# Performance work log

Measured on AMD Instinct MI355X. Metric: run time of the kernel, lower is better.

## Reference

```python
import jax, jax.numpy as jnp
import numpy as np

B, S, H, NH = 2, 2048, 1024, 16
HD = H // NH
INV_NORM = 1.0 / float(np.sqrt(HD))
BETA = 1.0


def setup_inputs() -> dict:
    key = jax.random.key(0)
    ks = jax.random.split(key, 8)
    causal = ~jnp.tril(jnp.ones((S, S), dtype=bool))  # True = masked (future)
    return {
        "hidden_states": jax.random.normal(ks[0], (B, S, H), dtype=jnp.float32),
        "residual": jax.random.normal(ks[1], (B, S, H), dtype=jnp.float32),
        "alibi": jax.random.normal(ks[2], (B * NH, 1, S), dtype=jnp.float32) * 0.1,
        "attention_mask": jnp.broadcast_to(causal[None, None], (B, 1, S, S)),
        "W_qkv": jax.random.normal(ks[3], (3 * H, H), dtype=jnp.float32) * (1.0 / np.sqrt(H)),
        "b_qkv": jax.random.normal(ks[4], (3 * H,), dtype=jnp.float32) * 0.02,
        "W_d": jax.random.normal(ks[5], (H, H), dtype=jnp.float32) * (1.0 / np.sqrt(H)),
        "b_d": jax.random.normal(ks[6], (H,), dtype=jnp.float32) * 0.02,
    }


def reference(hidden_states, residual, alibi, attention_mask, W_qkv, b_qkv, W_d, b_d):
    b, s, h = hidden_states.shape
    # fused QKV projection, split per-head interleaved [B,S,NH,3,HD]
    fused = hidden_states @ W_qkv.T + b_qkv
    fused = fused.reshape(b, s, NH, 3, HD)
    q = jnp.transpose(fused[..., 0, :], (0, 2, 1, 3))  # [B,NH,S,HD]
    k = jnp.transpose(fused[..., 1, :], (0, 2, 1, 3))
    v = jnp.transpose(fused[..., 2, :], (0, 2, 1, 3))
    # baddbmm: beta*alibi + alpha * q @ k^T
    scores = BETA * alibi.reshape(b, NH, 1, s) + INV_NORM * jnp.einsum(
        "bhqd,bhkd->bhqk", q, k
    )  # [B,NH,S,S]
    neg_min = jnp.finfo(scores.dtype).min
    scores = jnp.where(attention_mask, neg_min, scores)
    probs = jax.nn.softmax(scores.astype(jnp.float32), axis=-1).astype(scores.dtype)
    ctx = jnp.einsum("bhqk,bhkd->bhqd", probs, v)  # [B,NH,S,HD]
    ctx = jnp.transpose(ctx, (0, 2, 1, 3)).reshape(b, s, h)  # merge heads
    out = ctx @ W_d.T + b_d
    return residual + out  # dropout p=0
```

## Files before the change

### kernel.cpp

```cpp
#include <hip/hip_runtime.h>
#include <stdint.h>

#define BATCH 2
#define SLEN 2048
#define HDIM 1024
#define NH 16
#define HD 64
#define NHEADS 32
#define M_ROWS 4096
#define N_QKV 3072

typedef float f32x4 __attribute__((ext_vector_type(4)));
typedef float f32x16 __attribute__((ext_vector_type(16)));
typedef short bf16x8 __attribute__((ext_vector_type(8)));

typedef __attribute__((address_space(1))) unsigned int GU32;
typedef __attribute__((address_space(3))) unsigned int LU32;

__device__ __forceinline__ void gld16(const void* g, void* l) {
  __builtin_amdgcn_global_load_lds((GU32*)g, (LU32*)l, 16, 0, 0);
}

__device__ __forceinline__ unsigned short f2bf(float x) {
  union { float f; unsigned int u; } v; v.f = x;
  unsigned int r = v.u + 0x7fffu + ((v.u >> 16) & 1u);
  return (unsigned short)(r >> 16);
}

__device__ __forceinline__ float fexp2(float x) {
  float r; asm("v_exp_f32 %0, %1" : "=v"(r) : "v"(x)); return r;
}
__device__ __forceinline__ unsigned cvtpk(float lo, float hi) {
  unsigned r; asm("v_cvt_pk_bf16_f32 %0, %1, %2" : "=v"(r) : "v"(lo), "v"(hi)); return r;
}

#define MFMA32(a, b, c) __builtin_amdgcn_mfma_f32_32x32x16_bf16(a, b, c, 0, 0, 0)
#define MFMA16(a, b, c) __builtin_amdgcn_mfma_f32_16x16x32_bf16(a, b, c, 0, 0, 0)
#define ZERO16 {0.f,0.f,0.f,0.f,0.f,0.f,0.f,0.f,0.f,0.f,0.f,0.f,0.f,0.f,0.f,0.f}

__global__ void __launch_bounds__(256) k_prep(
    const float* __restrict__ hidden, const float* __restrict__ wqkv,
    const float* __restrict__ wd,
    unsigned short* __restrict__ hb, unsigned short* __restrict__ wqkb,
    unsigned short* __restrict__ wdb) {
  int bid = blockIdx.x;
  const float* src;
  unsigned short* dst;
  int i;
  if (bid < 4096)      { src = hidden; dst = hb;   i = bid * 256 + threadIdx.x; }
  else if (bid < 7168) { src = wqkv;  dst = wqkb;  i = (bid - 4096) * 256 + threadIdx.x; }
  else                 { src = wd;    dst = wdb;   i = (bid - 7168) * 256 + threadIdx.x; }
  float4 v = ((const float4*)src)[i];
  ushort4 o;
  o.x = f2bf(v.x); o.y = f2bf(v.y); o.z = f2bf(v.z); o.w = f2bf(v.w);
  ((ushort4*)dst)[i] = o;
}

__global__ void __launch_bounds__(256) k_gemm_qkv(
    const unsigned short* __restrict__ A,
    const unsigned short* __restrict__ Bw,
    const float* __restrict__ bias,
    unsigned short* __restrict__ Qo,
    unsigned short* __restrict__ Ko,
    unsigned short* __restrict__ Vto) {
  __shared__ __align__(16) unsigned short Alds[128 * 32];
  __shared__ __align__(16) unsigned short Blds[128 * 32];
  const int tid = threadIdx.x;
  const int w = tid >> 6, lane = tid & 63;
  const int g = lane >> 4, l15 = lane & 15;
  const int wr = w >> 1, wc = w & 1;
  const int tm = blockIdx.x * 128, tn = blockIdx.y * 128;

  const f32x4 zero = {0.f, 0.f, 0.f, 0.f};
  f32x4 acc[4][4];
#pragma unroll
  for (int m = 0; m < 4; ++m)
#pragma unroll
    for (int n = 0; n < 4; ++n) acc[m][n] = zero;

  for (int k0 = 0; k0 < 1024; k0 += 32) {
    __syncthreads();
#pragma unroll
    for (int r = 0; r < 2; ++r) {
      int c = r * 256 + w * 64 + lane;
      int row = c >> 2, cc = c & 3;
      gld16(A + (size_t)(tm + row) * 1024 + k0 + cc * 8,
            (char*)Alds + (r * 256 + w * 64) * 16);
      gld16(Bw + (size_t)(tn + row) * 1024 + k0 + cc * 8,
            (char*)Blds + (r * 256 + w * 64) * 16);
    }
    __syncthreads();
    bf16x8 af[4], bfv[4];
#pragma unroll
    for (int m = 0; m < 4; ++m)
      af[m] = *(const bf16x8*)(Alds + (wr * 64 + m * 16 + l15) * 32 + g * 8);
#pragma unroll
    for (int n = 0; n < 4; ++n)
      bfv[n] = *(const bf16x8*)(Blds + (wc * 64 + n * 16 + l15) * 32 + g * 8);
#pragma unroll
    for (int m = 0; m < 4; ++m)
#pragma unroll
      for (int n = 0; n < 4; ++n)
        acc[m][n] = MFMA16(af[m], bfv[n], acc[m][n]);
  }

#pragma unroll
  for (int n = 0; n < 4; ++n) {
    int col = tn + wc * 64 + n * 16 + l15;
    float bv = bias[col];
    int c6 = col >> 6;
    int nh = c6 / 3;
    int which = c6 - nh * 3;
    int hd = col & 63;
#pragma unroll
    for (int m = 0; m < 4; ++m) {
      int row0 = tm + wr * 64 + m * 16 + g * 4;
      int b = row0 >> 11;
      int s0 = row0 & 2047;
      int head = b * NH + nh;
      if (which == 2) {
        ushort4 pk;
        pk.x = f2bf(acc[m][n][0] + bv);
        pk.y = f2bf(acc[m][n][1] + bv);
        pk.z = f2bf(acc[m][n][2] + bv);
        pk.w = f2bf(acc[m][n][3] + bv);
        *(ushort4*)(Vto + ((size_t)head * HD + hd) * SLEN + s0) = pk;
      } else {
        unsigned short* dst = (which == 0) ? Qo : Ko;
        size_t base = (size_t)head * SLEN * HD;
#pragma unroll
        for (int j = 0; j < 4; ++j)
          dst[base + (size_t)(s0 + j) * HD + hd] = f2bf(acc[m][n][j] + bv);
      }
    }
  }
}

__global__ void __launch_bounds__(256) k_gemm_out(
    const unsigned short* __restrict__ A,
    const unsigned short* __restrict__ Bw,
    const float* __restrict__ bias,
    const float* __restrict__ residual,
    float* __restrict__ out) {
  __shared__ __align__(16) unsigned short Alds[128 * 32];
  __shared__ __align__(16) unsigned short Blds[64 * 32];
  const int tid = threadIdx.x;
  const int w = tid >> 6, lane = tid & 63;
  const int g = lane >> 4, l15 = lane & 15;
  const int wr = w >> 1, wc = w & 1;
  const int tm = blockIdx.x * 128, tn = blockIdx.y * 64;

  const f32x4 zero = {0.f, 0.f, 0.f, 0.f};
  f32x4 acc[4][2];
#pragma unroll
  for (int m = 0; m < 4; ++m)
#pragma unroll
    for (int n = 0; n < 2; ++n) acc[m][n] = zero;

  for (int k0 = 0; k0 < 1024; k0 += 32) {
    __syncthreads();
#pragma unroll
    for (int r = 0; r < 2; ++r) {
      int c = r * 256 + tid;
      int row = c >> 2, cc = c & 3;
      gld16(A + (size_t)(tm + row) * 1024 + k0 + cc * 8,
            (char*)Alds + c * 16);
    }
    {
      int row = tid >> 2, cc = tid & 3;
      gld16(Bw + (size_t)(tn + row) * 1024 + k0 + cc * 8,
            (char*)Blds + tid * 16);
    }
    __syncthreads();
    bf16x8 af[4], bfv[2];
#pragma unroll
    for (int m = 0; m < 4; ++m)
      af[m] = *(const bf16x8*)(Alds + (wr * 64 + m * 16 + l15) * 32 + g * 8);
#pragma unroll
    for (int n = 0; n < 2; ++n)
      bfv[n] = *(const bf16x8*)(Blds + (wc * 32 + n * 16 + l15) * 32 + g * 8);
#pragma unroll
    for (int m = 0; m < 4; ++m)
#pragma unroll
      for (int n = 0; n < 2; ++n)
        acc[m][n] = MFMA16(af[m], bfv[n], acc[m][n]);
  }

#pragma unroll
  for (int n = 0; n < 2; ++n) {
    int col = tn + wc * 32 + n * 16 + l15;
    float bv = bias[col];
#pragma unroll
    for (int m = 0; m < 4; ++m) {
      int row0 = tm + wr * 64 + m * 16 + g * 4;
#pragma unroll
      for (int j = 0; j < 4; ++j) {
        size_t idx = (size_t)(row0 + j) * 1024 + col;
        out[idx] = acc[m][n][j] + bv + residual[idx];
      }
    }
  }
}

__global__ void __launch_bounds__(512, 4) k_attn(
    const unsigned short* __restrict__ Q,
    const unsigned short* __restrict__ K,
    const unsigned short* __restrict__ Vt,
    const float* __restrict__ alibi,
    unsigned short* __restrict__ ctx) {
  __shared__ __align__(16) unsigned short Kl[2][2][64 * 64];
  __shared__ __align__(16) unsigned short Vl[2][2][64 * 64];
  __shared__ __align__(16) float Al[2048];

  const int n = blockIdx.x;
  const int head = n & 31;
  const int t = n >> 5;
  const int bq = (t < 8) ? (15 - t) : (t - 8);
  const int tid = threadIdx.x;
  const int w = tid >> 6, lane = tid & 63;
  const int l31 = lane & 31, h = lane >> 5;
  const int rsw = l31 & 7;
  const int qsub = w & 3, par = w >> 2;
  const int qw = bq * 128 + qsub * 32;
  const int ksd = 4 * bq + qsub;

  const unsigned short* Qh = Q + (size_t)head * SLEN * HD;
  const unsigned short* Kh = K + (size_t)head * SLEN * HD;
  const unsigned short* Vh = Vt + (size_t)head * HD * SLEN;

  bf16x8 qr0, qr1, qr2, qr3;
  {
    const unsigned short* qp = Qh + (size_t)(qw + l31) * HD + h * 8;
    qr0 = *(const bf16x8*)(qp);
    qr1 = *(const bf16x8*)(qp + 16);
    qr2 = *(const bf16x8*)(qp + 32);
    qr3 = *(const bf16x8*)(qp + 48);
  }

  f32x16 ot0 = ZERO16, ot1 = ZERO16;
  float m_run = -1e30f, l_acc = 0.f;
  const float C1 = 0.18033688011f;

#define STAGE(nb, itt)                                                          \
  do {                                                                          \
    const int kb_ = (2 * (itt)) * 64;                                           \
    const int row_ = tid >> 3;                                                  \
    const int sw_ = ((tid & 7) ^ (row_ & 7)) * 8;                               \
    gld16(Kh + (size_t)(kb_ + row_) * HD + sw_, (char*)&Kl[nb][0][0] + tid * 16);      \
    gld16(Kh + (size_t)(kb_ + 64 + row_) * HD + sw_, (char*)&Kl[nb][1][0] + tid * 16); \
    gld16(Vh + (size_t)row_ * SLEN + kb_ + sw_, (char*)&Vl[nb][0][0] + tid * 16);      \
    gld16(Vh + (size_t)row_ * SLEN + kb_ + 64 + sw_, (char*)&Vl[nb][1][0] + tid * 16); \
  } while (0)

  STAGE(0, 0);
  {
    float4 av = *(const float4*)(alibi + (size_t)head * SLEN + tid * 4);
    av.x *= 1.44269504f; av.y *= 1.44269504f;
    av.z *= 1.44269504f; av.w *= 1.44269504f;
    *(float4*)(Al + tid * 4) = av;
  }
  __syncthreads();
  int cur = 0;

  for (int it = 0; it <= bq; ++it) {
    if (it < bq) STAGE(cur ^ 1, it + 1);
    const int kt = 2 * it + par;
    const int ks0 = 2 * kt;
    if (ks0 <= ksd) {
      const char* kbase = (const char*)&Kl[cur][par][0];
      const char* vbase = (const char*)&Vl[cur][par][0];
      const bool hs1 = (ks0 + 1 <= ksd);

      f32x16 st[2];
      __builtin_amdgcn_s_setprio(1);
#pragma unroll
      for (int s = 0; s < 2; ++s) {
        if (s == 1 && !hs1) break;
        const char* kr = kbase + (s * 32 + l31) * 128;
        f32x16 a = ZERO16;
        a = MFMA32(*(const bf16x8*)(kr + (((0 + h) ^ rsw) * 16)), qr0, a);
        a = MFMA32(*(const bf16x8*)(kr + (((2 + h) ^ rsw) * 16)), qr1, a);
        a = MFMA32(*(const bf16x8*)(kr + (((4 + h) ^ rsw) * 16)), qr2, a);
        a = MFMA32(*(const bf16x8*)(kr + (((6 + h) ^ rsw) * 16)), qr3, a);
        st[s] = a;
      }
      __builtin_amdgcn_s_setprio(0);

#pragma unroll
      for (int s = 0; s < 2; ++s) {
        if (s == 1 && !hs1) break;
        const int ks = ks0 + s;
        const float* ab = Al + ks * 32 + 4 * h;
        f32x4 alq0 = *(const f32x4*)(ab);
        f32x4 alq1 = *(const f32x4*)(ab + 8);
        f32x4 alq2 = *(const f32x4*)(ab + 16);
        f32x4 alq3 = *(const f32x4*)(ab + 24);

        float p[16];
#pragma unroll
        for (int i = 0; i < 4; ++i) {
          p[i]      = st[s][i]      * C1 + alq0[i];
          p[4 + i]  = st[s][4 + i]  * C1 + alq1[i];
          p[8 + i]  = st[s][8 + i]  * C1 + alq2[i];
          p[12 + i] = st[s][12 + i] * C1 + alq3[i];
        }
        if (ks == ksd) {
#pragma unroll
          for (int i = 0; i < 16; ++i) {
            int krow = (i & 3) + 8 * (i >> 2) + 4 * h;
            p[i] = (krow > l31) ? -1e30f : p[i];
          }
        }
        float m01 = fmaxf(p[0], p[1]),  m23 = fmaxf(p[2], p[3]);
        float m45 = fmaxf(p[4], p[5]),  m67 = fmaxf(p[6], p[7]);
        float m89 = fmaxf(p[8], p[9]),  mab = fmaxf(p[10], p[11]);
        float mcd = fmaxf(p[12], p[13]), mef = fmaxf(p[14], p[15]);
        float pm = fmaxf(fmaxf(fmaxf(m01, m23), fmaxf(m45, m67)),
                         fmaxf(fmaxf(m89, mab), fmaxf(mcd, mef)));
        pm = fmaxf(pm, __shfl_xor(pm, 32));
        if (!__all(pm <= m_run + 8.0f)) {
          float mnew = fmaxf(m_run, pm);
          float sc = fexp2(m_run - mnew);
          m_run = mnew;
          l_acc *= sc;
          ot0 *= sc;
          ot1 *= sc;
        }
        float e[16];
        float ss = 0.f;
#pragma unroll
        for (int i = 0; i < 16; ++i) { e[i] = fexp2(p[i] - m_run); ss += e[i]; }
        l_acc += ss;

        unsigned a0 = cvtpk(e[0], e[1]),   a1 = cvtpk(e[2], e[3]);
        unsigned a2 = cvtpk(e[4], e[5]),   a3 = cvtpk(e[6], e[7]);
        unsigned b0 = cvtpk(e[8], e[9]),   b1 = cvtpk(e[10], e[11]);
        unsigned b2 = cvtpk(e[12], e[13]), b3 = cvtpk(e[14], e[15]);
        unsigned t0 = h ? a0 : a2, t1 = h ? a1 : a3;
        unsigned t2 = h ? b0 : b2, t3 = h ? b1 : b3;
        unsigned r0 = __shfl_xor(t0, 32), r1 = __shfl_xor(t1, 32);
        unsigned r2 = __shfl_xor(t2, 32), r3 = __shfl_xor(t3, 32);
        union { unsigned u[4]; bf16x8 v; } P0, P1;
        P0.u[0] = h ? r0 : a0;  P0.u[1] = h ? r1 : a1;
        P0.u[2] = h ? a2 : r0;  P0.u[3] = h ? a3 : r1;
        P1.u[0] = h ? r2 : b0;  P1.u[1] = h ? r3 : b1;
        P1.u[2] = h ? b2 : r2;  P1.u[3] = h ? b3 : r3;

        __builtin_amdgcn_s_setprio(1);
        {
          const char* vr0 = vbase + l31 * 128;
          const char* vr1 = vbase + (32 + l31) * 128;
          bf16x8 vf;
          vf = *(const bf16x8*)(vr0 + (((4 * s + 0 + h) ^ rsw) * 16)); ot0 = MFMA32(vf, P0.v, ot0);
          vf = *(const bf16x8*)(vr0 + (((4 * s + 2 + h) ^ rsw) * 16)); ot0 = MFMA32(vf, P1.v, ot0);
          vf = *(const bf16x8*)(vr1 + (((4 * s + 0 + h) ^ rsw) * 16)); ot1 = MFMA32(vf, P0.v, ot1);
          vf = *(const bf16x8*)(vr1 + (((4 * s + 2 + h) ^ rsw) * 16)); ot1 = MFMA32(vf, P1.v, ot1);
        }
        __builtin_amdgcn_s_setprio(0);
      }
    }
    __syncthreads();
    cur ^= 1;
  }
#undef STAGE

  float* Ob = (float*)&Kl[0][0][0];
  float* Mb = (float*)&Vl[0][0][0];
  const int idx = qsub * 64 + lane;
  const int xs = idx & 7;
  float* op = Ob + (size_t)idx * 32;
  if (par == 1) {
#pragma unroll
    for (int c = 0; c < 4; ++c) {
      f32x4 t2 = {ot0[4 * c], ot0[4 * c + 1], ot0[4 * c + 2], ot0[4 * c + 3]};
      *(f32x4*)(op + ((c ^ xs) * 4)) = t2;
      f32x4 u = {ot1[4 * c], ot1[4 * c + 1], ot1[4 * c + 2], ot1[4 * c + 3]};
      *(f32x4*)(op + (((c + 4) ^ xs) * 4)) = u;
    }
    Mb[idx * 2] = m_run;
    Mb[idx * 2 + 1] = l_acc;
  }
  __syncthreads();
  if (par == 0) {
    float m1 = Mb[idx * 2], l1 = Mb[idx * 2 + 1];
    float mt = fmaxf(m_run, m1);
    float s0 = fexp2(m_run - mt), s1 = fexp2(m1 - mt);
    float lme = l_acc * s0 + l1 * s1;
    float ltot = lme + __shfl_xor(lme, 32);
    float inv = 1.0f / ltot;
#pragma unroll
    for (int c = 0; c < 4; ++c) {
      f32x4 t2 = *(const f32x4*)(op + ((c ^ xs) * 4));
      f32x4 u = *(const f32x4*)(op + (((c + 4) ^ xs) * 4));
#pragma unroll
      for (int j = 0; j < 4; ++j) {
        ot0[4 * c + j] = ot0[4 * c + j] * s0 + t2[j] * s1;
        ot1[4 * c + j] = ot1[4 * c + j] * s0 + u[j] * s1;
      }
    }
    const int b = head >> 4, nh = head & 15;
    unsigned short* cb = ctx + ((size_t)b * SLEN + qw + l31) * HDIM + nh * HD + 4 * h;
#pragma unroll
    for (int rg = 0; rg < 4; ++rg) {
      ushort4 o;
      o.x = f2bf(ot0[4 * rg + 0] * inv);
      o.y = f2bf(ot0[4 * rg + 1] * inv);
      o.z = f2bf(ot0[4 * rg + 2] * inv);
      o.w = f2bf(ot0[4 * rg + 3] * inv);
      *(ushort4*)(cb + 8 * rg) = o;
      o.x = f2bf(ot1[4 * rg + 0] * inv);
      o.y = f2bf(ot1[4 * rg + 1] * inv);
      o.z = f2bf(ot1[4 * rg + 2] * inv);
      o.w = f2bf(ot1[4 * rg + 3] * inv);
      *(ushort4*)(cb + 32 + 8 * rg) = o;
    }
  }
}

extern "C" void kernel_launch(void* const* d_in, const int* in_sizes, int n_in,
                              void* d_out, int out_size, void* d_ws, size_t ws_size,
                              hipStream_t stream) {
  const float* hidden   = (const float*)d_in[0];
  const float* residual = (const float*)d_in[1];
  const float* alibi    = (const float*)d_in[2];
  const float* W_qkv = (const float*)d_in[4];
  const float* b_qkv = (const float*)d_in[5];
  const float* W_d   = (const float*)d_in[6];
  const float* b_d   = (const float*)d_in[7];
  float* out = (float*)d_out;

  unsigned short* hb   = (unsigned short*)d_ws;
  unsigned short* wqkb = hb + (size_t)M_ROWS * HDIM;
  unsigned short* wdb  = wqkb + (size_t)N_QKV * HDIM;
  unsigned short* Qb   = wdb + (size_t)HDIM * HDIM;
  unsigned short* Kb   = Qb + (size_t)NHEADS * SLEN * HD;
  unsigned short* Vtb  = Kb + (size_t)NHEADS * SLEN * HD;
  unsigned short* ctxb = Vtb + (size_t)NHEADS * SLEN * HD;

  k_prep<<<dim3(8192), dim3(256), 0, stream>>>(hidden, W_qkv, W_d, hb, wqkb, wdb);
  k_gemm_qkv<<<dim3(32, 24), dim3(256), 0, stream>>>(hb, wqkb, b_qkv, Qb, Kb, Vtb);
  k_attn<<<dim3(512), dim3(512), 0, stream>>>(Qb, Kb, Vtb, alibi, ctxb);
  k_gemm_out<<<dim3(32, 16), dim3(256), 0, stream>>>(ctxb, wdb, b_d, residual, out);
}
```

Measured before the change: 104.2 us.

## Rewrite QKV GEMM with 256x256 tiles, double-buffered swizzled LDS and interleaved prefetch

The QKV projection GEMM moves from 128x128 tiles with a single-buffered 32-wide K loop to 256x256 tiles computed by 8 waves over 64-wide K steps. A and B tiles are double-buffered in LDS with an XOR swizzle, and global-to-LDS loads for the next step are interleaved with MFMA clusters using explicit barriers, vmcnt waits and setprio. The aim is to hide load latency and cut LDS bank conflicts. In exchange the large tiles use 128KB of LDS and yield only 192 blocks, which may leave CUs idle.

```diff
diff --git a/kernel.cpp b/kernel.cpp
--- a/kernel.cpp
+++ b/kernel.cpp
@@ -37,6 +37,10 @@
 #define MFMA32(a, b, c) __builtin_amdgcn_mfma_f32_32x32x16_bf16(a, b, c, 0, 0, 0)
 #define MFMA16(a, b, c) __builtin_amdgcn_mfma_f32_16x16x32_bf16(a, b, c, 0, 0, 0)
 #define ZERO16 {0.f,0.f,0.f,0.f,0.f,0.f,0.f,0.f,0.f,0.f,0.f,0.f,0.f,0.f,0.f,0.f}
+
+#define FENCE asm volatile("" ::: "memory")
+#define BAR do { FENCE; __builtin_amdgcn_s_barrier(); FENCE; } while (0)
+#define VMCNT(n) asm volatile("s_waitcnt vmcnt(" #n ")" ::: "memory")
 
 __global__ void __launch_bounds__(256) k_prep(
     const float* __restrict__ hidden, const float* __restrict__ wqkv,
@@ -56,65 +60,124 @@
   ((ushort4*)dst)[i] = o;
 }
 
-__global__ void __launch_bounds__(256) k_gemm_qkv(
+__global__ void __launch_bounds__(512, 2) k_gemm_qkv(
     const unsigned short* __restrict__ A,
     const unsigned short* __restrict__ Bw,
     const float* __restrict__ bias,
     unsigned short* __restrict__ Qo,
     unsigned short* __restrict__ Ko,
     unsigned short* __restrict__ Vto) {
-  __shared__ __align__(16) unsigned short Alds[128 * 32];
-  __shared__ __align__(16) unsigned short Blds[128 * 32];
+  __shared__ __align__(16) unsigned short Al_[2][256 * 64];
+  __shared__ __align__(16) unsigned short Bl_[2][256 * 64];
   const int tid = threadIdx.x;
   const int w = tid >> 6, lane = tid & 63;
   const int g = lane >> 4, l15 = lane & 15;
-  const int wr = w >> 1, wc = w & 1;
-  const int tm = blockIdx.x * 128, tn = blockIdx.y * 128;
+  const int wr = w >> 2, wn = w & 3;
+  const int tm = blockIdx.x * 256, tn = blockIdx.y * 256;
+  const int srow = tid >> 3, slot = tid & 7;
+
+#define STAGE_H(ldsbase, gsrc)                                                        \
+  do {                                                                                \
+    const unsigned short* g0_ = (gsrc) + (size_t)srow * 1024;                         \
+    gld16(g0_ + ((slot ^ (srow & 7)) * 8), (char*)(ldsbase) + (srow * 8 + slot) * 16); \
+    const unsigned short* g1_ = (gsrc) + (size_t)(srow + 64) * 1024;                  \
+    gld16(g1_ + ((slot ^ (srow & 7)) * 8), (char*)(ldsbase) + ((srow + 64) * 8 + slot) * 16); \
+  } while (0)
+
+#define LOAD_APAIR(q)                                                     \
+  do {                                                                    \
+    _Pragma("unroll")                                                     \
+    for (int i = 0; i < 2; ++i) {                                         \
+      int row = wr * 128 + (2 * (q) + i) * 16 + l15;                      \
+      const char* rb = (const char*)Ab + row * 128;                       \
+      int sw = row & 7;                                                   \
+      af[i][0] = *(const bf16x8*)(rb + ((g ^ sw) * 16));                  \
+      af[i][1] = *(const bf16x8*)(rb + (((4 + g) ^ sw) * 16));            \
+    }                                                                     \
+  } while (0)
+
+#define MFMA_PAIR(q)                                                      \
+  do {                                                                    \
+    __builtin_amdgcn_s_setprio(1);                                        \
+    _Pragma("unroll")                                                     \
+    for (int i = 0; i < 2; ++i) {                                         \
+      _Pragma("unroll")                                                   \
+      for (int n = 0; n < 4; ++n) {                                       \
+        acc[2 * (q) + i][n] = MFMA16(af[i][0], bfr[n][0], acc[2 * (q) + i][n]); \
+        acc[2 * (q) + i][n] = MFMA16(af[i][1], bfr[n][1], acc[2 * (q) + i][n]); \
+      }                                                                   \
+    }                                                                     \
+    __builtin_amdgcn_s_setprio(0);                                        \
+  } while (0)
 
   const f32x4 zero = {0.f, 0.f, 0.f, 0.f};
-  f32x4 acc[4][4];
-#pragma unroll
-  for (int m = 0; m < 4; ++m)
+  f32x4 acc[8][4];
+#pragma unroll
+  for (int m = 0; m < 8; ++m)
 #pragma unroll
     for (int n = 0; n < 4; ++n) acc[m][n] = zero;
 
-  for (int k0 = 0; k0 < 1024; k0 += 32) {
-    __syncthreads();
-#pragma unroll
-    for (int r = 0; r < 2; ++r) {
-      int c = r * 256 + w * 64 + lane;
-      int row = c >> 2, cc = c & 3;
-      gld16(A + (size_t)(tm + row) * 1024 + k0 + cc * 8,
-            (char*)Alds + (r * 256 + w * 64) * 16);
-      gld16(Bw + (size_t)(tn + row) * 1024 + k0 + cc * 8,
-            (char*)Blds + (r * 256 + w * 64) * 16);
-    }
-    __syncthreads();
-    bf16x8 af[4], bfv[4];
-#pragma unroll
-    for (int m = 0; m < 4; ++m)
-      af[m] = *(const bf16x8*)(Alds + (wr * 64 + m * 16 + l15) * 32 + g * 8);
-#pragma unroll
-    for (int n = 0; n < 4; ++n)
-      bfv[n] = *(const bf16x8*)(Blds + (wc * 64 + n * 16 + l15) * 32 + g * 8);
-#pragma unroll
-    for (int m = 0; m < 4; ++m)
-#pragma unroll
-      for (int n = 0; n < 4; ++n)
-        acc[m][n] = MFMA16(af[m], bfv[n], acc[m][n]);
-  }
+  STAGE_H(Bl_[0], Bw + (size_t)tn * 1024);
+  STAGE_H((unsigned short*)Bl_[0] + 128 * 64, Bw + (size_t)(tn + 128) * 1024);
+  STAGE_H(Al_[0], A + (size_t)tm * 1024);
+  STAGE_H((unsigned short*)Al_[0] + 128 * 64, A + (size_t)(tm + 128) * 1024);
+  STAGE_H(Bl_[1], Bw + (size_t)tn * 1024 + 64);
+  STAGE_H((unsigned short*)Bl_[1] + 128 * 64, Bw + (size_t)(tn + 128) * 1024 + 64);
+  VMCNT(4);
+  BAR;
+
+  for (int t = 0; t < 16; ++t) {
+    const int p = t & 1;
+    const unsigned short* Ab = Al_[p];
+    const unsigned short* Bb = Bl_[p];
+    const int kn0 = (t + 1) * 64, kn1 = (t + 2) * 64;
+    bf16x8 bfr[4][2];
+    bf16x8 af[2][2];
+#pragma unroll
+    for (int n = 0; n < 4; ++n) {
+      int row = wn * 64 + n * 16 + l15;
+      const char* rb = (const char*)Bb + row * 128;
+      int sw = row & 7;
+      bfr[n][0] = *(const bf16x8*)(rb + ((g ^ sw) * 16));
+      bfr[n][1] = *(const bf16x8*)(rb + (((4 + g) ^ sw) * 16));
+    }
+    LOAD_APAIR(0);
+    if (t < 15) STAGE_H(Al_[p ^ 1], A + (size_t)tm * 1024 + kn0);
+    BAR;
+    MFMA_PAIR(0);
+    BAR;
+    LOAD_APAIR(1);
+    if (t < 15) STAGE_H((unsigned short*)Al_[p ^ 1] + 128 * 64, A + (size_t)(tm + 128) * 1024 + kn0);
+    if (t < 14) STAGE_H(Bl_[p], Bw + (size_t)tn * 1024 + kn1);
+    BAR;
+    MFMA_PAIR(1);
+    BAR;
+    LOAD_APAIR(2);
+    if (t < 14) STAGE_H((unsigned short*)Bl_[p] + 128 * 64, Bw + (size_t)(tn + 128) * 1024 + kn1);
+    BAR;
+    MFMA_PAIR(2);
+    BAR;
+    LOAD_APAIR(3);
+    BAR;
+    MFMA_PAIR(3);
+    if (t < 14) { VMCNT(4); } else if (t == 14) { VMCNT(0); }
+    BAR;
+  }
+#undef STAGE_H
+#undef LOAD_APAIR
+#undef MFMA_PAIR
 
 #pragma unroll
   for (int n = 0; n < 4; ++n) {
-    int col = tn + wc * 64 + n * 16 + l15;
+    int col = tn + wn * 64 + n * 16 + l15;
     float bv = bias[col];
     int c6 = col >> 6;
     int nh = c6 / 3;
     int which = c6 - nh * 3;
     int hd = col & 63;
 #pragma unroll
-    for (int m = 0; m < 4; ++m) {
-      int row0 = tm + wr * 64 + m * 16 + g * 4;
+    for (int m = 0; m < 8; ++m) {
+      int row0 = tm + wr * 128 + m * 16 + g * 4;
       int b = row0 >> 11;
       int s0 = row0 & 2047;
       int head = b * NH + nh;
@@ -438,7 +501,7 @@
   unsigned short* ctxb = Vtb + (size_t)NHEADS * SLEN * HD;
 
   k_prep<<<dim3(8192), dim3(256), 0, stream>>>(hidden, W_qkv, W_d, hb, wqkb, wdb);
-  k_gemm_qkv<<<dim3(32, 24), dim3(256), 0, stream>>>(hb, wqkb, b_qkv, Qb, Kb, Vtb);
+  k_gemm_qkv<<<dim3(16, 12), dim3(512), 0, stream>>>(hb, wqkb, b_qkv, Qb, Kb, Vtb);
   k_attn<<<dim3(512), dim3(512), 0, stream>>>(Qb, Kb, Vtb, alibi, ctxb);
   k_gemm_out<<<dim3(32, 16), dim3(256), 0, stream>>>(ctxb, wdb, b_d, residual, out);
 }
```

After: 110.5 us. 1.06x slower.

## Halve attention K/V stage size to 64 keys and raise occupancy

Applied to the files above, without the earlier changes.

The attention kernel now stages one 64-key K/V tile per iteration instead of two. Each wave parity handles a 32-key half of that tile, and the kernel runs twice as many iterations. Shared memory shrinks from about 72KB to 40KB, and launch bounds ask for 8 blocks per CU, so more workgroups can be resident and hide latency. The cost is twice as many __syncthreads barriers and staging rounds, and less work per barrier.

```diff
diff --git a/kernel.cpp b/kernel.cpp
--- a/kernel.cpp
+++ b/kernel.cpp
@@ -202,15 +202,16 @@
   }
 }
 
-__global__ void __launch_bounds__(512, 4) k_attn(
+__global__ void __launch_bounds__(512, 8) k_attn(
     const unsigned short* __restrict__ Q,
     const unsigned short* __restrict__ K,
     const unsigned short* __restrict__ Vt,
     const float* __restrict__ alibi,
     unsigned short* __restrict__ ctx) {
-  __shared__ __align__(16) unsigned short Kl[2][2][64 * 64];
-  __shared__ __align__(16) unsigned short Vl[2][2][64 * 64];
-  __shared__ __align__(16) float Al[2048];
+  __shared__ __align__(16) char Lbuf[40960];
+  unsigned short* KlB = (unsigned short*)Lbuf;
+  unsigned short* VlB = (unsigned short*)(Lbuf + 16384);
+  float* Al = (float*)(Lbuf + 32768);
 
   const int n = blockIdx.x;
   const int head = n & 31;
@@ -243,13 +244,11 @@
 
 #define STAGE(nb, itt)                                                          \
   do {                                                                          \
-    const int kb_ = (2 * (itt)) * 64;                                           \
+    const int kb_ = (itt) * 64;                                                 \
     const int row_ = tid >> 3;                                                  \
     const int sw_ = ((tid & 7) ^ (row_ & 7)) * 8;                               \
-    gld16(Kh + (size_t)(kb_ + row_) * HD + sw_, (char*)&Kl[nb][0][0] + tid * 16);      \
-    gld16(Kh + (size_t)(kb_ + 64 + row_) * HD + sw_, (char*)&Kl[nb][1][0] + tid * 16); \
-    gld16(Vh + (size_t)row_ * SLEN + kb_ + sw_, (char*)&Vl[nb][0][0] + tid * 16);      \
-    gld16(Vh + (size_t)row_ * SLEN + kb_ + 64 + sw_, (char*)&Vl[nb][1][0] + tid * 16); \
+    gld16(Kh + (size_t)(kb_ + row_) * HD + sw_, (char*)(KlB + (nb) * 4096) + tid * 16); \
+    gld16(Vh + (size_t)row_ * SLEN + kb_ + sw_, (char*)(VlB + (nb) * 4096) + tid * 16); \
   } while (0)
 
   STAGE(0, 0);
@@ -261,111 +260,101 @@
   }
   __syncthreads();
   int cur = 0;
-
-  for (int it = 0; it <= bq; ++it) {
-    if (it < bq) STAGE(cur ^ 1, it + 1);
-    const int kt = 2 * it + par;
-    const int ks0 = 2 * kt;
-    if (ks0 <= ksd) {
-      const char* kbase = (const char*)&Kl[cur][par][0];
-      const char* vbase = (const char*)&Vl[cur][par][0];
-      const bool hs1 = (ks0 + 1 <= ksd);
-
-      f32x16 st[2];
+  const int itmax = 2 * bq + 2;
+
+  for (int it = 0; it < itmax; ++it) {
+    if (it + 1 < itmax) STAGE(cur ^ 1, it + 1);
+    const int ks = 2 * it + par;
+    if (ks <= ksd) {
+      const char* kbase = (const char*)(KlB + cur * 4096);
+      const char* vbase = (const char*)(VlB + cur * 4096);
+
+      f32x16 st = ZERO16;
       __builtin_amdgcn_s_setprio(1);
-#pragma unroll
-      for (int s = 0; s < 2; ++s) {
-        if (s == 1 && !hs1) break;
-        const char* kr = kbase + (s * 32 + l31) * 128;
-        f32x16 a = ZERO16;
-        a = MFMA32(*(const bf16x8*)(kr + (((0 + h) ^ rsw) * 16)), qr0, a);
-        a = MFMA32(*(const bf16x8*)(kr + (((2 + h) ^ rsw) * 16)), qr1, a);
-        a = MFMA32(*(const bf16x8*)(kr + (((4 + h) ^ rsw) * 16)), qr2, a);
-        a = MFMA32(*(const bf16x8*)(kr + (((6 + h) ^ rsw) * 16)), qr3, a);
-        st[s] = a;
+      {
+        const char* kr = kbase + (par * 32 + l31) * 128;
+        st = MFMA32(*(const bf16x8*)(kr + (((0 + h) ^ rsw) * 16)), qr0, st);
+        st = MFMA32(*(const bf16x8*)(kr + (((2 + h) ^ rsw) * 16)), qr1, st);
+        st = MFMA32(*(const bf16x8*)(kr + (((4 + h) ^ rsw) * 16)), qr2, st);
+        st = MFMA32(*(const bf16x8*)(kr + (((6 + h) ^ rsw) * 16)), qr3, st);
       }
       __builtin_amdgcn_s_setprio(0);
 
-#pragma unroll
-      for (int s = 0; s < 2; ++s) {
-        if (s == 1 && !hs1) break;
-        const int ks = ks0 + s;
-        const float* ab = Al + ks * 32 + 4 * h;
-        f32x4 alq0 = *(const f32x4*)(ab);
-        f32x4 alq1 = *(const f32x4*)(ab + 8);
-        f32x4 alq2 = *(const f32x4*)(ab + 16);
-        f32x4 alq3 = *(const f32x4*)(ab + 24);
-
-        float p[16];
-#pragma unroll
-        for (int i = 0; i < 4; ++i) {
-          p[i]      = st[s][i]      * C1 + alq0[i];
-          p[4 + i]  = st[s][4 + i]  * C1 + alq1[i];
-          p[8 + i]  = st[s][8 + i]  * C1 + alq2[i];
-          p[12 + i] = st[s][12 + i] * C1 + alq3[i];
+      const float* ab = Al + ks * 32 + 4 * h;
+      f32x4 alq0 = *(const f32x4*)(ab);
+      f32x4 alq1 = *(const f32x4*)(ab + 8);
+      f32x4 alq2 = *(const f32x4*)(ab + 16);
+      f32x4 alq3 = *(const f32x4*)(ab + 24);
+
+      float p[16];
+#pragma unroll
+      for (int i = 0; i < 4; ++i) {
+        p[i]      = st[i]      * C1 + alq0[i];
+        p[4 + i]  = st[4 + i]  * C1 + alq1[i];
+        p[8 + i]  = st[8 + i]  * C1 + alq2[i];
+        p[12 + i] = st[12 + i] * C1 + alq3[i];
+      }
+      if (ks == ksd) {
+#pragma unroll
+        for (int i = 0; i < 16; ++i) {
+          int krow = (i & 3) + 8 * (i >> 2) + 4 * h;
+          p[i] = (krow > l31) ? -1e30f : p[i];
         }
-        if (ks == ksd) {
-#pragma unroll
-          for (int i = 0; i < 16; ++i) {
-            int krow = (i & 3) + 8 * (i >> 2) + 4 * h;
-            p[i] = (krow > l31) ? -1e30f : p[i];
-          }
-        }
-        float m01 = fmaxf(p[0], p[1]),  m23 = fmaxf(p[2], p[3]);
-        float m45 = fmaxf(p[4], p[5]),  m67 = fmaxf(p[6], p[7]);
-        float m89 = fmaxf(p[8], p[9]),  mab = fmaxf(p[10], p[11]);
-        float mcd = fmaxf(p[12], p[13]), mef = fmaxf(p[14], p[15]);
-        float pm = fmaxf(fmaxf(fmaxf(m01, m23), fmaxf(m45, m67)),
-                         fmaxf(fmaxf(m89, mab), fmaxf(mcd, mef)));
-        pm = fmaxf(pm, __shfl_xor(pm, 32));
-        if (!__all(pm <= m_run + 8.0f)) {
-          float mnew = fmaxf(m_run, pm);
-          float sc = fexp2(m_run - mnew);
-          m_run = mnew;
-          l_acc *= sc;
-          ot0 *= sc;
-          ot1 *= sc;
-        }
-        float e[16];
-        float ss = 0.f;
-#pragma unroll
-        for (int i = 0; i < 16; ++i) { e[i] = fexp2(p[i] - m_run); ss += e[i]; }
-        l_acc += ss;
-
-        unsigned a0 = cvtpk(e[0], e[1]),   a1 = cvtpk(e[2], e[3]);
-        unsigned a2 = cvtpk(e[4], e[5]),   a3 = cvtpk(e[6], e[7]);
-        unsigned b0 = cvtpk(e[8], e[9]),   b1 = cvtpk(e[10], e[11]);
-        unsigned b2 = cvtpk(e[12], e[13]), b3 = cvtpk(e[14], e[15]);
-        unsigned t0 = h ? a0 : a2, t1 = h ? a1 : a3;
-        unsigned t2 = h ? b0 : b2, t3 = h ? b1 : b3;
-        unsigned r0 = __shfl_xor(t0, 32), r1 = __shfl_xor(t1, 32);
-        unsigned r2 = __shfl_xor(t2, 32), r3 = __shfl_xor(t3, 32);
-        union { unsigned u[4]; bf16x8 v; } P0, P1;
-        P0.u[0] = h ? r0 : a0;  P0.u[1] = h ? r1 : a1;
-        P0.u[2] = h ? a2 : r0;  P0.u[3] = h ? a3 : r1;
-        P1.u[0] = h ? r2 : b0;  P1.u[1] = h ? r3 : b1;
-        P1.u[2] = h ? b2 : r2;  P1.u[3] = h ? b3 : r3;
-
-        __builtin_amdgcn_s_setprio(1);
-        {
-          const char* vr0 = vbase + l31 * 128;
-          const char* vr1 = vbase + (32 + l31) * 128;
-          bf16x8 vf;
-          vf = *(const bf16x8*)(vr0 + (((4 * s + 0 + h) ^ rsw) * 16)); ot0 = MFMA32(vf, P0.v, ot0);
-          vf = *(const bf16x8*)(vr0 + (((4 * s + 2 + h) ^ rsw) * 16)); ot0 = MFMA32(vf, P1.v, ot0);
-          vf = *(const bf16x8*)(vr1 + (((4 * s + 0 + h) ^ rsw) * 16)); ot1 = MFMA32(vf, P0.v, ot1);
-          vf = *(const bf16x8*)(vr1 + (((4 * s + 2 + h) ^ rsw) * 16)); ot1 = MFMA32(vf, P1.v, ot1);
-        }
-        __builtin_amdgcn_s_setprio(0);
-      }
+      }
+      float x0 = fmaxf(fmaxf(p[0], p[1]), p[2]);
+      float x1 = fmaxf(fmaxf(p[3], p[4]), p[5]);
+      float x2 = fmaxf(fmaxf(p[6], p[7]), p[8]);
+      float x3 = fmaxf(fmaxf(p[9], p[10]), p[11]);
+      float x4 = fmaxf(fmaxf(p[12], p[13]), p[14]);
+      float pm = fmaxf(fmaxf(fmaxf(x0, x1), x2), fmaxf(fmaxf(x3, x4), p[15]));
+      pm = fmaxf(pm, __shfl_xor(pm, 32));
+      if (!__all(pm <= m_run + 8.0f)) {
+        float mnew = fmaxf(m_run, pm);
+        float sc = fexp2(m_run - mnew);
+        m_run = mnew;
+        l_acc *= sc;
+        ot0 *= sc;
+        ot1 *= sc;
+      }
+      float e[16];
+      float ss = 0.f;
+#pragma unroll
+      for (int i = 0; i < 16; ++i) { e[i] = fexp2(p[i] - m_run); ss += e[i]; }
+      l_acc += ss;
+
+      unsigned a0 = cvtpk(e[0], e[1]),   a1 = cvtpk(e[2], e[3]);
+      unsigned a2 = cvtpk(e[4], e[5]),   a3 = cvtpk(e[6], e[7]);
+      unsigned b0 = cvtpk(e[8], e[9]),   b1 = cvtpk(e[10], e[11]);
+      unsigned b2 = cvtpk(e[12], e[13]), b3 = cvtpk(e[14], e[15]);
+      unsigned t0 = h ? a0 : a2, t1 = h ? a1 : a3;
+      unsigned t2 = h ? b0 : b2, t3 = h ? b1 : b3;
+      unsigned r0 = __shfl_xor(t0, 32), r1 = __shfl_xor(t1, 32);
+      unsigned r2 = __shfl_xor(t2, 32), r3 = __shfl_xor(t3, 32);
+      union { unsigned u[4]; bf16x8 v; } P0, P1;
+      P0.u[0] = h ? r0 : a0;  P0.u[1] = h ? r1 : a1;
+      P0.u[2] = h ? a2 : r0;  P0.u[3] = h ? a3 : r1;
+      P1.u[0] = h ? r2 : b0;  P1.u[1] = h ? r3 : b1;
+      P1.u[2] = h ? b2 : r2;  P1.u[3] = h ? b3 : r3;
+
+      __builtin_amdgcn_s_setprio(1);
+      {
+        const char* vr0 = vbase + l31 * 128;
+        const char* vr1 = vbase + (32 + l31) * 128;
+        bf16x8 vf;
+        vf = *(const bf16x8*)(vr0 + (((4 * par + 0 + h) ^ rsw) * 16)); ot0 = MFMA32(vf, P0.v, ot0);
+        vf = *(const bf16x8*)(vr0 + (((4 * par + 2 + h) ^ rsw) * 16)); ot0 = MFMA32(vf, P1.v, ot0);
+        vf = *(const bf16x8*)(vr1 + (((4 * par + 0 + h) ^ rsw) * 16)); ot1 = MFMA32(vf, P0.v, ot1);
+        vf = *(const bf16x8*)(vr1 + (((4 * par + 2 + h) ^ rsw) * 16)); ot1 = MFMA32(vf, P1.v, ot1);
+      }
+      __builtin_amdgcn_s_setprio(0);
     }
     __syncthreads();
     cur ^= 1;
   }
 #undef STAGE
 
-  float* Ob = (float*)&Kl[0][0][0];
-  float* Mb = (float*)&Vl[0][0][0];
+  float* Ob = (float*)Lbuf;
+  float* Mb = (float*)(Lbuf + 32768);
   const int idx = qsub * 64 + lane;
   const int xs = idx & 7;
   float* op = Ob + (size_t)idx * 32;
```

After: 265.4 us. +154.7%, slower.
